# Kernel tuning notes

Hardware: AMD Instinct MI355X
Metric: run time of the kernel (lower is better)

Reference implementation:

```python
import jax, jax.numpy as jnp
import numpy as np

D_MODEL = 1024
NUM_HEADS = 16
HEAD_DIM = D_MODEL // NUM_HEADS
D_FF = 4 * D_MODEL


def _linear_params(key, d_in, d_out):
    kw, kb = jax.random.split(key)
    bound = 1.0 / np.sqrt(d_in)
    W = jax.random.uniform(kw, (d_in, d_out), minval=-bound, maxval=bound, dtype=jnp.float32)
    b = jax.random.uniform(kb, (d_out,), minval=-bound, maxval=bound, dtype=jnp.float32)
    return W, b


def setup_inputs() -> dict:
    key = jax.random.key(0)
    ks = jax.random.split(key, 6)
    x = jax.random.normal(ks[0], (4, 2048, D_MODEL), dtype=jnp.float32)
    qkv_w, qkv_b = _linear_params(ks[1], D_MODEL, 3 * D_MODEL)
    out_w, out_b = _linear_params(ks[2], D_MODEL, D_MODEL)
    ffn1_w, ffn1_b = _linear_params(ks[3], D_MODEL, D_FF)
    ffn2_w, ffn2_b = _linear_params(ks[4], D_FF, D_MODEL)
    ln1_g = jnp.ones((D_MODEL,), jnp.float32); ln1_b = jnp.zeros((D_MODEL,), jnp.float32)
    ln2_g = jnp.ones((D_MODEL,), jnp.float32); ln2_b = jnp.zeros((D_MODEL,), jnp.float32)
    return {
        "x": x,
        "qkv_w": qkv_w, "qkv_b": qkv_b,
        "out_w": out_w, "out_b": out_b,
        "ffn1_w": ffn1_w, "ffn1_b": ffn1_b,
        "ffn2_w": ffn2_w, "ffn2_b": ffn2_b,
        "ln1_g": ln1_g, "ln1_b": ln1_b,
        "ln2_g": ln2_g, "ln2_b": ln2_b,
    }


def _layer_norm(x, g, b, eps=1e-5):
    mu = jnp.mean(x, axis=-1, keepdims=True)
    var = jnp.mean(jnp.square(x - mu), axis=-1, keepdims=True)
    return (x - mu) * jax.lax.rsqrt(var + eps) * g + b


def reference(x, qkv_w, qkv_b, out_w, out_b, ffn1_w, ffn1_b, ffn2_w, ffn2_b,
              ln1_g, ln1_b, ln2_g, ln2_b):
    B, S, D = x.shape
    H, Hd = NUM_HEADS, HEAD_DIM
    normed = _layer_norm(x, ln1_g, ln1_b)
    qkv = normed @ qkv_w + qkv_b                      # [B,S,3D]
    qkv = qkv.reshape(B, S, 3, H, Hd)
    q = jnp.transpose(qkv[:, :, 0], (0, 2, 1, 3))     # [B,H,S,Hd]
    k = jnp.transpose(qkv[:, :, 1], (0, 2, 1, 3))
    v = jnp.transpose(qkv[:, :, 2], (0, 2, 1, 3))
    scores = jnp.einsum('bhqd,bhkd->bhqk', q, k) / np.sqrt(Hd).astype(np.float32)
    causal = jnp.tril(jnp.ones((S, S), dtype=bool))
    scores = jnp.where(causal[None, None], scores, -jnp.inf)
    attn = jax.nn.softmax(scores, axis=-1)
    attn_out = jnp.einsum('bhqk,bhkd->bhqd', attn, v)  # [B,H,S,Hd]
    attn_out = jnp.transpose(attn_out, (0, 2, 1, 3)).reshape(B, S, D)
    attn_out = attn_out @ out_w + out_b
    x = x + attn_out
    h = _layer_norm(x, ln2_g, ln2_b)
    h = jax.nn.gelu(h @ ffn1_w + ffn1_b, approximate=False)
    h = h @ ffn2_w + ffn2_b
    return x + h
```

## Files before the change

### kernel.cpp

```cpp
#include <hip/hip_runtime.h>
#include <hip/hip_bf16.h>
#include <math.h>

typedef __attribute__((ext_vector_type(8))) short short8;
typedef __attribute__((ext_vector_type(4))) float f32x4;

__device__ __forceinline__ float bf2f(unsigned short u) {
    union { unsigned int i; float f; } c; c.i = ((unsigned int)u) << 16; return c.f;
}
__device__ __forceinline__ unsigned short f2bf(float f) {
    union { float f; unsigned int i; } c; c.f = f;
    unsigned int i = c.i;
    unsigned int r = (i + 0x7FFFu + ((i >> 16) & 1u)) >> 16;
    return (unsigned short)r;
}
__device__ __forceinline__ float fexp2(float x) { return __builtin_amdgcn_exp2f(x); }

__device__ __forceinline__ void load8(const unsigned short* p, float* v) {
    short8 s = *(const short8*)p;
#pragma unroll
    for (int i = 0; i < 8; i++) v[i] = bf2f((unsigned short)s[i]);
}
__device__ __forceinline__ void load8(const float* p, float* v) {
    f32x4 a = ((const f32x4*)p)[0], b = ((const f32x4*)p)[1];
    v[0] = a[0]; v[1] = a[1]; v[2] = a[2]; v[3] = a[3];
    v[4] = b[0]; v[5] = b[1]; v[6] = b[2]; v[7] = b[3];
}
__device__ __forceinline__ void store8(unsigned short* p, const float* v) {
    short8 s;
#pragma unroll
    for (int i = 0; i < 8; i++) s[i] = (short)f2bf(v[i]);
    *(short8*)p = s;
}
__device__ __forceinline__ void store8(float* p, const float* v) {
    f32x4 a, b;
    a[0] = v[0]; a[1] = v[1]; a[2] = v[2]; a[3] = v[3];
    b[0] = v[4]; b[1] = v[5]; b[2] = v[6]; b[3] = v[7];
    ((f32x4*)p)[0] = a; ((f32x4*)p)[1] = b;
}

__global__ __launch_bounds__(256) void ln_f32_kernel(
    const float* __restrict__ x, const float* __restrict__ g,
    const float* __restrict__ b, unsigned short* __restrict__ out) {
    const int row = blockIdx.x;
    const int t = threadIdx.x;
    const float* xr = x + (size_t)row * 1024;
    float4 raw = ((const float4*)xr)[t];
    float v0 = raw.x, v1 = raw.y, v2 = raw.z, v3 = raw.w;
    float s = v0 + v1 + v2 + v3;
    float ss = v0 * v0 + v1 * v1 + v2 * v2 + v3 * v3;
    for (int off = 32; off > 0; off >>= 1) {
        s += __shfl_down(s, off);
        ss += __shfl_down(ss, off);
    }
    __shared__ float red[8];
    __shared__ float stat[2];
    const int wave = t >> 6, lane = t & 63;
    if (lane == 0) { red[wave] = s; red[4 + wave] = ss; }
    __syncthreads();
    if (t == 0) {
        float st = red[0] + red[1] + red[2] + red[3];
        float sst = red[4] + red[5] + red[6] + red[7];
        float mu = st * (1.0f / 1024.0f);
        float var = sst * (1.0f / 1024.0f) - mu * mu;
        stat[0] = mu; stat[1] = rsqrtf(var + 1e-5f);
    }
    __syncthreads();
    const float mu = stat[0], rstd = stat[1];
    float4 gr = ((const float4*)g)[t];
    float4 br = ((const float4*)b)[t];
    ushort4 o;
    o.x = f2bf((v0 - mu) * rstd * gr.x + br.x);
    o.y = f2bf((v1 - mu) * rstd * gr.y + br.y);
    o.z = f2bf((v2 - mu) * rstd * gr.z + br.z);
    o.w = f2bf((v3 - mu) * rstd * gr.w + br.w);
    ((ushort4*)(out + (size_t)row * 1024))[t] = o;
}

__global__ __launch_bounds__(256) void ln_bf16_kernel(
    const unsigned short* __restrict__ x, const float* __restrict__ g,
    const float* __restrict__ b, unsigned short* __restrict__ out) {
    const int row = blockIdx.x;
    const int t = threadIdx.x;
    const unsigned short* xr = x + (size_t)row * 1024;
    ushort4 raw = ((const ushort4*)xr)[t];
    float v0 = bf2f(raw.x), v1 = bf2f(raw.y), v2 = bf2f(raw.z), v3 = bf2f(raw.w);
    float s = v0 + v1 + v2 + v3;
    float ss = v0 * v0 + v1 * v1 + v2 * v2 + v3 * v3;
    for (int off = 32; off > 0; off >>= 1) {
        s += __shfl_down(s, off);
        ss += __shfl_down(ss, off);
    }
    __shared__ float red[8];
    __shared__ float stat[2];
    const int wave = t >> 6, lane = t & 63;
    if (lane == 0) { red[wave] = s; red[4 + wave] = ss; }
    __syncthreads();
    if (t == 0) {
        float st = red[0] + red[1] + red[2] + red[3];
        float sst = red[4] + red[5] + red[6] + red[7];
        float mu = st * (1.0f / 1024.0f);
        float var = sst * (1.0f / 1024.0f) - mu * mu;
        stat[0] = mu; stat[1] = rsqrtf(var + 1e-5f);
    }
    __syncthreads();
    const float mu = stat[0], rstd = stat[1];
    float4 gr = ((const float4*)g)[t];
    float4 br = ((const float4*)b)[t];
    ushort4 o;
    o.x = f2bf((v0 - mu) * rstd * gr.x + br.x);
    o.y = f2bf((v1 - mu) * rstd * gr.y + br.y);
    o.z = f2bf((v2 - mu) * rstd * gr.z + br.z);
    o.w = f2bf((v3 - mu) * rstd * gr.w + br.w);
    ((ushort4*)(out + (size_t)row * 1024))[t] = o;
}

__global__ __launch_bounds__(256) void transpose_cast_kernel(
    const float* __restrict__ in, unsigned short* __restrict__ out, int R, int C) {
    __shared__ unsigned short tile[32][33];
    const int bx = blockIdx.x * 32, by = blockIdx.y * 32;
    const int tx = threadIdx.x & 31, ty = threadIdx.x >> 5;
    for (int i = 0; i < 32; i += 8)
        tile[ty + i][tx] = f2bf(in[(size_t)(by + ty + i) * C + bx + tx]);
    __syncthreads();
    for (int i = 0; i < 32; i += 8)
        out[(size_t)(bx + ty + i) * R + by + tx] = tile[tx][ty + i];
}

enum { EPI_QKV = 0, EPI_RES = 1, EPI_GELU = 2 };

template <int EPI, typename RT, typename OT>
__global__ __launch_bounds__(256) void gemm_bt(
    const unsigned short* __restrict__ A, const unsigned short* __restrict__ Bt,
    const float* __restrict__ bias, const RT* __restrict__ res,
    OT* __restrict__ o0, unsigned short* __restrict__ o1,
    unsigned short* __restrict__ o2, int M, int N, int K) {
    constexpr int LDW = 40;
    constexpr int LE = 136;
    __shared__ __align__(16) unsigned short SMEM[20480];
    const int t = threadIdx.x;
    const int wave = t >> 6, lane = t & 63;
    const int lr = lane & 15, lq = lane >> 4;
    const int wm = (wave >> 1) * 64, wn = (wave & 1) * 64;
    const int m0 = blockIdx.y * 128, n0 = blockIdx.x * 128;
    f32x4 acc[4][4] = {};
    const int arow = t >> 2, acol = (t & 3) << 3;
    const unsigned short* ag = A + (size_t)(m0 + arow) * K + acol;
    const unsigned short* bg = Bt + (size_t)(n0 + arow) * K + acol;
    const size_t rstride = (size_t)64 * K;
    short8 a0 = *(const short8*)(ag);
    short8 a1 = *(const short8*)(ag + rstride);
    short8 b0 = *(const short8*)(bg);
    short8 b1 = *(const short8*)(bg + rstride);
    const int nit = K >> 5;
    for (int it = 0; it < nit; ++it) {
        const int buf = (it & 1) * 10240;
        unsigned short* As = SMEM + buf;
        unsigned short* Bs = SMEM + buf + 5120;
        *(short8*)(As + arow * LDW + acol) = a0;
        *(short8*)(As + (arow + 64) * LDW + acol) = a1;
        *(short8*)(Bs + arow * LDW + acol) = b0;
        *(short8*)(Bs + (arow + 64) * LDW + acol) = b1;
        if (it + 1 < nit) {
            const int k0 = (it + 1) << 5;
            a0 = *(const short8*)(ag + k0);
            a1 = *(const short8*)(ag + rstride + k0);
            b0 = *(const short8*)(bg + k0);
            b1 = *(const short8*)(bg + rstride + k0);
        }
        __syncthreads();
        short8 af[4], bfr[4];
#pragma unroll
        for (int i = 0; i < 4; i++) af[i] = *(const short8*)(As + (wm + i * 16 + lr) * LDW + lq * 8);
#pragma unroll
        for (int i = 0; i < 4; i++) bfr[i] = *(const short8*)(Bs + (wn + i * 16 + lr) * LDW + lq * 8);
#pragma unroll
        for (int mi = 0; mi < 4; mi++)
#pragma unroll
            for (int ni = 0; ni < 4; ni++)
                acc[mi][ni] = __builtin_amdgcn_mfma_f32_16x16x32_bf16(af[mi], bfr[ni], acc[mi][ni], 0, 0, 0);
    }
    __syncthreads();
    const bool vreg = (EPI == EPI_QKV) && (n0 >= 2048);
#pragma unroll
    for (int ni = 0; ni < 4; ni++) {
        const int col = wn + ni * 16 + lr;
        const float bv = bias[n0 + col];
#pragma unroll
        for (int mi = 0; mi < 4; mi++) {
#pragma unroll
            for (int r = 0; r < 4; r++) {
                const int row = wm + mi * 16 + lq * 4 + r;
                float val = acc[mi][ni][r] + bv;
                if (EPI == EPI_GELU)
                    val = 0.5f * val * (1.0f + erff(val * 0.70710678118654752f));
                if (vreg) SMEM[col * LE + row] = f2bf(val);
                else      SMEM[row * LE + col] = f2bf(val);
            }
        }
    }
    __syncthreads();
    const int rr = t >> 1, half = (t & 1) * 64;
    if (EPI == EPI_RES || EPI == EPI_GELU) {
        const size_t base = (size_t)(m0 + rr) * N + n0 + half;
        const unsigned short* src = SMEM + rr * LE + half;
#pragma unroll
        for (int j = 0; j < 8; j++) {
            float v[8];
            load8(src + j * 8, v);
            if (EPI == EPI_RES) {
                float rv[8];
                load8(res + base + j * 8, rv);
#pragma unroll
                for (int i = 0; i < 8; i++) v[i] += rv[i];
            }
            store8(o0 + base + j * 8, v);
        }
    } else if (!vreg) {
        const int gcol0 = n0 + half;
        const int which = gcol0 >> 10;
        const int hn = (gcol0 & 1023) >> 6;
        const int grow = m0 + rr;
        const size_t bh = (size_t)((grow >> 11) * 16 + hn);
        unsigned short* dst = (which == 0) ? (unsigned short*)o0 : o1;
        dst += (bh * 2048 + (grow & 2047)) * 64;
        const unsigned short* src = SMEM + rr * LE + half;
#pragma unroll
        for (int j = 0; j < 8; j++)
            *(short8*)(dst + j * 8) = *(const short8*)(src + j * 8);
    } else {
        const int c = rr;
        const int rem = (n0 + c) - 2048;
        const int hn = rem >> 6, d = rem & 63;
        const size_t bh = (size_t)((m0 >> 11) * 16 + hn);
        unsigned short* dst = o2 + (bh * 64 + d) * 2048 + (m0 & 2047) + half;
        const unsigned short* src = SMEM + c * LE + half;
#pragma unroll
        for (int j = 0; j < 8; j++)
            *(short8*)(dst + j * 8) = *(const short8*)(src + j * 8);
    }
}

__global__ __launch_bounds__(256) void attn_kernel(
    const unsigned short* __restrict__ qb, const unsigned short* __restrict__ kb,
    const unsigned short* __restrict__ vtb, unsigned short* __restrict__ aout) {
    const int bx = blockIdx.x;
    const int bh = blockIdx.y;
    const int bidx = bh >> 4, h = bh & 15;
    const int t = threadIdx.x, wave = t >> 6, lane = t & 63;
    const int lr = lane & 15, lq = lane >> 4;
    __shared__ __align__(16) unsigned short Ks[64 * 68];
    __shared__ __align__(16) unsigned short Vs[64 * 68];
    __shared__ __align__(16) unsigned short Ps[4][32 * 68];
    const unsigned short* kbase = kb + (size_t)bh * 2048 * 64;
    const unsigned short* vbase = vtb + (size_t)bh * 64 * 2048;
    const int srow = t >> 3, scol = (t & 7) * 8;
    const float kQScale = 0.125f * 1.44269504088896f;

    for (int phase = 0; phase < 2; phase++) {
        const int qblk = phase ? (15 - bx) : bx;
        const unsigned short* qbase = qb + ((size_t)bh * 2048 + qblk * 128 + wave * 32) * 64;
        short8 qf[2][2];
#pragma unroll
        for (int f = 0; f < 2; f++)
#pragma unroll
            for (int c = 0; c < 2; c++) {
                short8 raw = *(const short8*)(qbase + (f * 16 + lr) * 64 + c * 32 + lq * 8);
                short8 sc;
#pragma unroll
                for (int j = 0; j < 8; j++)
                    sc[j] = (short)f2bf(bf2f((unsigned short)raw[j]) * kQScale);
                qf[f][c] = sc;
            }
        f32x4 acc[2][4] = {};
        float m_i[2][4], l_i[2][4];
#pragma unroll
        for (int f = 0; f < 2; f++)
#pragma unroll
            for (int r = 0; r < 4; r++) { m_i[f][r] = -1e30f; l_i[f][r] = 0.0f; }
        const int wave_q0 = qblk * 128 + wave * 32;
        const int nkt = 2 * (qblk + 1);
        short8 kr0 = *(const short8*)(kbase + t * 8);
        short8 kr1 = *(const short8*)(kbase + 2048 + t * 8);
        short8 vr0 = *(const short8*)(vbase + (size_t)srow * 2048 + scol);
        short8 vr1 = *(const short8*)(vbase + (size_t)(32 + srow) * 2048 + scol);
        for (int kt = 0; kt < nkt; kt++) {
            __syncthreads();
            *(short8*)(Ks + srow * 68 + scol) = kr0;
            *(short8*)(Ks + (32 + srow) * 68 + scol) = kr1;
            *(short8*)(Vs + srow * 68 + scol) = vr0;
            *(short8*)(Vs + (32 + srow) * 68 + scol) = vr1;
            __syncthreads();
            if (kt + 1 < nkt) {
                const unsigned short* kg = kbase + (kt + 1) * 4096;
                kr0 = *(const short8*)(kg + t * 8);
                kr1 = *(const short8*)(kg + 2048 + t * 8);
                vr0 = *(const short8*)(vbase + (size_t)srow * 2048 + (kt + 1) * 64 + scol);
                vr1 = *(const short8*)(vbase + (size_t)(32 + srow) * 2048 + (kt + 1) * 64 + scol);
            }
            if (kt * 64 <= wave_q0 + 31) {
                f32x4 sa[2][4];
#pragma unroll
                for (int ni = 0; ni < 4; ni++) {
                    short8 kf0 = *(const short8*)(Ks + (ni * 16 + lr) * 68 + lq * 8);
                    short8 kf1 = *(const short8*)(Ks + (ni * 16 + lr) * 68 + 32 + lq * 8);
#pragma unroll
                    for (int f = 0; f < 2; f++) {
                        f32x4 z = {};
                        z = __builtin_amdgcn_mfma_f32_16x16x32_bf16(qf[f][0], kf0, z, 0, 0, 0);
                        sa[f][ni] = __builtin_amdgcn_mfma_f32_16x16x32_bf16(qf[f][1], kf1, z, 0, 0, 0);
                    }
                }
                const bool needmask = (kt * 64 + 63 > wave_q0);
                if (needmask) {
#pragma unroll
                    for (int f = 0; f < 2; f++) {
                        const int qrow0 = wave_q0 + f * 16 + lq * 4;
#pragma unroll
                        for (int ni = 0; ni < 4; ni++) {
                            const int kcol = kt * 64 + ni * 16 + lr;
#pragma unroll
                            for (int r = 0; r < 4; r++)
                                if (kcol > qrow0 + r) sa[f][ni][r] = -1e30f;
                        }
                    }
                }
#pragma unroll
                for (int f = 0; f < 2; f++) {
                    float mcur[4], alpha[4], rsum[4];
#pragma unroll
                    for (int r = 0; r < 4; r++)
                        mcur[r] = fmaxf(fmaxf(sa[f][0][r], sa[f][1][r]), fmaxf(sa[f][2][r], sa[f][3][r]));
#pragma unroll
                    for (int r = 0; r < 4; r++) {
#pragma unroll
                        for (int off = 1; off < 16; off <<= 1) mcur[r] = fmaxf(mcur[r], __shfl_xor(mcur[r], off));
                        const float mn = fmaxf(m_i[f][r], mcur[r]);
                        alpha[r] = fexp2(m_i[f][r] - mn);
                        m_i[f][r] = mn;
                        rsum[r] = 0.0f;
                    }
#pragma unroll
                    for (int ni = 0; ni < 4; ni++)
#pragma unroll
                        for (int r = 0; r < 4; r++) {
                            const float p = fexp2(sa[f][ni][r] - m_i[f][r]);
                            Ps[wave][(f * 16 + lq * 4 + r) * 68 + ni * 16 + lr] = f2bf(p);
                            rsum[r] += p;
                        }
#pragma unroll
                    for (int r = 0; r < 4; r++) {
#pragma unroll
                        for (int off = 1; off < 16; off <<= 1) rsum[r] += __shfl_xor(rsum[r], off);
                        l_i[f][r] = l_i[f][r] * alpha[r] + rsum[r];
#pragma unroll
                        for (int ni = 0; ni < 4; ni++) acc[f][ni][r] *= alpha[r];
                    }
                }
                short8 pf[2][2];
#pragma unroll
                for (int f = 0; f < 2; f++)
#pragma unroll
                    for (int c = 0; c < 2; c++)
                        pf[f][c] = *(const short8*)(&Ps[wave][(f * 16 + lr) * 68 + c * 32 + lq * 8]);
#pragma unroll
                for (int ni = 0; ni < 4; ni++) {
                    short8 vf0 = *(const short8*)(Vs + (ni * 16 + lr) * 68 + lq * 8);
                    short8 vf1 = *(const short8*)(Vs + (ni * 16 + lr) * 68 + 32 + lq * 8);
#pragma unroll
                    for (int f = 0; f < 2; f++) {
                        acc[f][ni] = __builtin_amdgcn_mfma_f32_16x16x32_bf16(pf[f][0], vf0, acc[f][ni], 0, 0, 0);
                        acc[f][ni] = __builtin_amdgcn_mfma_f32_16x16x32_bf16(pf[f][1], vf1, acc[f][ni], 0, 0, 0);
                    }
                }
            }
        }
#pragma unroll
        for (int f = 0; f < 2; f++)
#pragma unroll
            for (int r = 0; r < 4; r++) {
                const float rinv = 1.0f / l_i[f][r];
                const int q = qblk * 128 + wave * 32 + f * 16 + lq * 4 + r;
                const size_t token = (size_t)bidx * 2048 + q;
#pragma unroll
                for (int ni = 0; ni < 4; ni++)
                    aout[token * 1024 + h * 64 + ni * 16 + lr] = f2bf(acc[f][ni][r] * rinv);
            }
    }
}

extern "C" void kernel_launch(void* const* d_in, const int* in_sizes, int n_in,
                              void* d_out, int out_size, void* d_ws, size_t ws_size,
                              hipStream_t stream) {
    const float* x      = (const float*)d_in[0];
    const float* qkv_w  = (const float*)d_in[1];
    const float* qkv_b  = (const float*)d_in[2];
    const float* out_w  = (const float*)d_in[3];
    const float* out_b  = (const float*)d_in[4];
    const float* ffn1_w = (const float*)d_in[5];
    const float* ffn1_b = (const float*)d_in[6];
    const float* ffn2_w = (const float*)d_in[7];
    const float* ffn2_b = (const float*)d_in[8];
    const float* ln1_g  = (const float*)d_in[9];
    const float* ln1_b  = (const float*)d_in[10];
    const float* ln2_g  = (const float*)d_in[11];
    const float* ln2_b  = (const float*)d_in[12];
    float* out = (float*)d_out;
    char* W = (char*)d_ws;

    unsigned short* normed = (unsigned short*)(W);
    unsigned short* x1     = (unsigned short*)(W + 16777216);
    unsigned short* qbuf   = (unsigned short*)(W + 33554432);
    unsigned short* kbuf   = (unsigned short*)(W + 50331648);
    unsigned short* vbuf   = (unsigned short*)(W + 67108864);
    unsigned short* attnb  = (unsigned short*)(W + 83886080);
    unsigned short* hff    = (unsigned short*)(W + 33554432);
    unsigned short* qkv_wt = (unsigned short*)(W + 100663296);
    unsigned short* out_wt = (unsigned short*)(W + 106954752);
    unsigned short* f1_wt  = (unsigned short*)(W + 109051904);
    unsigned short* f2_wt  = (unsigned short*)(W + 117440512);

    transpose_cast_kernel<<<dim3(3072 / 32, 1024 / 32), 256, 0, stream>>>(qkv_w, qkv_wt, 1024, 3072);
    transpose_cast_kernel<<<dim3(1024 / 32, 1024 / 32), 256, 0, stream>>>(out_w, out_wt, 1024, 1024);
    transpose_cast_kernel<<<dim3(4096 / 32, 1024 / 32), 256, 0, stream>>>(ffn1_w, f1_wt, 1024, 4096);
    transpose_cast_kernel<<<dim3(1024 / 32, 4096 / 32), 256, 0, stream>>>(ffn2_w, f2_wt, 4096, 1024);

    ln_f32_kernel<<<dim3(8192), 256, 0, stream>>>(x, ln1_g, ln1_b, normed);
    gemm_bt<EPI_QKV, float, unsigned short><<<dim3(3072 / 128, 8192 / 128), 256, 0, stream>>>(
        normed, qkv_wt, qkv_b, nullptr, qbuf, kbuf, vbuf, 8192, 3072, 1024);
    attn_kernel<<<dim3(8, 64), 256, 0, stream>>>(qbuf, kbuf, vbuf, attnb);
    gemm_bt<EPI_RES, float, unsigned short><<<dim3(1024 / 128, 8192 / 128), 256, 0, stream>>>(
        attnb, out_wt, out_b, x, x1, nullptr, nullptr, 8192, 1024, 1024);
    ln_bf16_kernel<<<dim3(8192), 256, 0, stream>>>(x1, ln2_g, ln2_b, normed);
    gemm_bt<EPI_GELU, float, unsigned short><<<dim3(4096 / 128, 8192 / 128), 256, 0, stream>>>(
        normed, f1_wt, ffn1_b, nullptr, hff, nullptr, nullptr, 8192, 4096, 1024);
    gemm_bt<EPI_RES, unsigned short, float><<<dim3(1024 / 128, 8192 / 128), 256, 0, stream>>>(
        hff, f2_wt, ffn2_b, x1, out, nullptr, nullptr, 8192, 1024, 4096);
}
```

Measured before the change: 590.2 us.

## Stage GEMM tiles with direct global-to-LDS loads instead of register staging

The bf16 GEMM now copies A and B tiles straight from global memory into LDS with global_load_lds 16-byte transfers, instead of loading into registers and then writing to shared memory. The prefetch of the next K-slice goes into the alternate buffer right after the barrier, overlapping with MFMA work on the current buffer. This removes the register round-trip and the explicit LDS stores, and frees VGPRs. In exchange the LDS rows lose their padding (stride 32 instead of 40), so fragment reads may hit bank conflicts, and correctness relies on the compiler waiting for the asynchronous LDS writes before the barrier.

```diff
diff --git a/kernel.cpp b/kernel.cpp
--- a/kernel.cpp
+++ b/kernel.cpp
@@ -15,6 +15,12 @@
     return (unsigned short)r;
 }
 __device__ __forceinline__ float fexp2(float x) { return __builtin_amdgcn_exp2f(x); }
+
+__device__ __forceinline__ void gload16(const unsigned short* g, unsigned short* l) {
+    __builtin_amdgcn_global_load_lds(
+        (const __attribute__((address_space(1))) unsigned int*)g,
+        (__attribute__((address_space(3))) unsigned int*)l, 16, 0, 0);
+}
 
 __device__ __forceinline__ void load8(const unsigned short* p, float* v) {
     short8 s = *(const short8*)p;
@@ -135,9 +141,8 @@
     const float* __restrict__ bias, const RT* __restrict__ res,
     OT* __restrict__ o0, unsigned short* __restrict__ o1,
     unsigned short* __restrict__ o2, int M, int N, int K) {
-    constexpr int LDW = 40;
     constexpr int LE = 136;
-    __shared__ __align__(16) unsigned short SMEM[20480];
+    __shared__ __align__(16) unsigned short SMEM[17408];
     const int t = threadIdx.x;
     const int wave = t >> 6, lane = t & 63;
     const int lr = lane & 15, lq = lane >> 4;
@@ -148,32 +153,35 @@
     const unsigned short* ag = A + (size_t)(m0 + arow) * K + acol;
     const unsigned short* bg = Bt + (size_t)(n0 + arow) * K + acol;
     const size_t rstride = (size_t)64 * K;
-    short8 a0 = *(const short8*)(ag);
-    short8 a1 = *(const short8*)(ag + rstride);
-    short8 b0 = *(const short8*)(bg);
-    short8 b1 = *(const short8*)(bg + rstride);
+    const int t8 = t * 8;
+    {
+        unsigned short* As = SMEM;
+        unsigned short* Bs = SMEM + 4096;
+        gload16(ag, As + t8);
+        gload16(ag + rstride, As + 2048 + t8);
+        gload16(bg, Bs + t8);
+        gload16(bg + rstride, Bs + 2048 + t8);
+    }
     const int nit = K >> 5;
     for (int it = 0; it < nit; ++it) {
-        const int buf = (it & 1) * 10240;
-        unsigned short* As = SMEM + buf;
-        unsigned short* Bs = SMEM + buf + 5120;
-        *(short8*)(As + arow * LDW + acol) = a0;
-        *(short8*)(As + (arow + 64) * LDW + acol) = a1;
-        *(short8*)(Bs + arow * LDW + acol) = b0;
-        *(short8*)(Bs + (arow + 64) * LDW + acol) = b1;
+        __syncthreads();
         if (it + 1 < nit) {
+            const int nbuf = ((it + 1) & 1) * 8192;
             const int k0 = (it + 1) << 5;
-            a0 = *(const short8*)(ag + k0);
-            a1 = *(const short8*)(ag + rstride + k0);
-            b0 = *(const short8*)(bg + k0);
-            b1 = *(const short8*)(bg + rstride + k0);
+            unsigned short* As = SMEM + nbuf;
+            unsigned short* Bs = SMEM + nbuf + 4096;
+            gload16(ag + k0, As + t8);
+            gload16(ag + rstride + k0, As + 2048 + t8);
+            gload16(bg + k0, Bs + t8);
+            gload16(bg + rstride + k0, Bs + 2048 + t8);
         }
-        __syncthreads();
+        const unsigned short* As = SMEM + (it & 1) * 8192;
+        const unsigned short* Bs = As + 4096;
         short8 af[4], bfr[4];
 #pragma unroll
-        for (int i = 0; i < 4; i++) af[i] = *(const short8*)(As + (wm + i * 16 + lr) * LDW + lq * 8);
-#pragma unroll
-        for (int i = 0; i < 4; i++) bfr[i] = *(const short8*)(Bs + (wn + i * 16 + lr) * LDW + lq * 8);
+        for (int i = 0; i < 4; i++) af[i] = *(const short8*)(As + (wm + i * 16 + lr) * 32 + lq * 8);
+#pragma unroll
+        for (int i = 0; i < 4; i++) bfr[i] = *(const short8*)(Bs + (wn + i * 16 + lr) * 32 + lq * 8);
 #pragma unroll
         for (int mi = 0; mi < 4; mi++)
 #pragma unroll
```

New measurement: 604.8 us. +2.5%, slower.
